# Kernel tuning notes

Measured on AMD Instinct MI355X. Metric: run time of the kernel, lower is better.

## Reference

```python
import jax, jax.numpy as jnp
import numpy as np

MD = 4                  # corr_md
D = 2 * MD + 1          # patch_size = 9


def setup_inputs() -> dict:
    key = jax.random.key(0)
    k1, k2 = jax.random.split(key)
    b, c, h, w = 4, 128, 128, 256
    t1 = jax.random.normal(k1, (b, c, h, w), dtype=jnp.float32)
    t2 = jax.random.normal(k2, (b, c, h, w), dtype=jnp.float32)
    return {"t1": t1, "t2": t2}


def reference(t1, t2):
    # Local cost volume: for each displacement (di, dj) in [-MD, MD]^2,
    # out[b, p, y, x] = sum_c t1[b, c, y, x] * t2[b, c, y+di, x+dj]
    # with zero padding outside t2 (SpatialCorrelationSampler semantics,
    # kernel_size=1, stride=1, dilation_patch=1; no channel normalization).
    b, c, h, w = t1.shape
    t2p = jnp.pad(t2, ((0, 0), (0, 0), (MD, MD), (MD, MD)))
    # Loop over the fixed 9x9 displacement grid (81 small reductions);
    outs = [
        jnp.einsum('bchw,bchw->bhw', t1, t2p[:, :, i:i + h, j:j + w])
        for i in range(D) for j in range(D)
    ]
    return jnp.stack(outs, axis=1)  # [b, 81, h, w]
```

## Files before the change

### kernel.cpp

```cpp
#include <hip/hip_runtime.h>

#define NP 81
#define CC 128
#define HH 128
#define WW 256
#define TX 64

typedef __attribute__((ext_vector_type(8))) short short8;
typedef __attribute__((ext_vector_type(4))) float f32x4;

__device__ __forceinline__ short f2bf(float f) {
    unsigned int u = __builtin_bit_cast(unsigned int, f);
    u += 0x7fffu + ((u >> 16) & 1u);
    return (short)(u >> 16);
}

__global__ __launch_bounds__(256) void corr_mfma_kernel(
        const float* __restrict__ t1, const float* __restrict__ t2,
        float* __restrict__ out) {
    const int id = blockIdx.x;
    const int xt = id & 3;
    const int y  = (id >> 2) & (HH - 1);
    const int b  = id >> 9;
    const int X0 = xt * TX;

    const int tid  = threadIdx.x;
    const int lane = tid & 63;
    const int wv   = tid >> 6;
    const int n    = lane & 15;
    const int q    = lane >> 4;

    __shared__ short smem[2560 + 28800];
    short* sA = smem;
    short* sB = smem + 2560;

    f32x4 acc[9][2];
#pragma unroll
    for (int i = 0; i < 9; i++)
#pragma unroll
        for (int t = 0; t < 2; t++) acc[i][t] = (f32x4){0.f, 0.f, 0.f, 0.f};

    const size_t plane = (size_t)HH * WW;
    const float* t1b = t1 + (size_t)b * CC * plane + (size_t)y * WW;
    const float* t2b = t2 + (size_t)b * CC * plane;

    for (int c0 = 0; c0 < CC; c0 += 32) {
        __syncthreads();
        {
            const int x  = tid & 63;
            const int cg = tid >> 6;
            const float* p = t1b + (size_t)(c0 + cg * 8) * plane + X0 + x;
            short8 pk;
#pragma unroll
            for (int j = 0; j < 8; j++) pk[j] = f2bf(p[(size_t)j * plane]);
            *(short8*)&sA[x * 40 + cg * 8] = pk;
        }
#pragma unroll
        for (int i = 0; i < 12; i++) {
            const int u = tid + i * 256;
            if (u < 2880) {
                const int r   = u / 320;
                const int rem = u - r * 320;
                const int cg  = rem / 80;
                const int ix  = rem - cg * 80;
                const int y2  = y + r - 4;
                const int x2  = X0 - 4 + ix;
                short8 pk;
                if (y2 >= 0 && y2 < HH && x2 >= 0 && x2 < WW) {
                    const float* p = t2b + (size_t)(c0 + cg * 8) * plane
                                   + (size_t)y2 * WW + x2;
#pragma unroll
                    for (int j = 0; j < 8; j++) pk[j] = f2bf(p[(size_t)j * plane]);
                } else {
#pragma unroll
                    for (int j = 0; j < 8; j++) pk[j] = 0;
                }
                *(short8*)&sB[r * 3200 + ix * 40 + cg * 8] = pk;
            }
        }
        __syncthreads();
        const short8 af = *(const short8*)&sA[(16 * wv + n) * 40 + q * 8];
#pragma unroll
        for (int di = 0; di < 9; di++) {
#pragma unroll
            for (int t = 0; t < 2; t++) {
                const short8 bf = *(const short8*)
                    &sB[di * 3200 + (16 * wv + 16 * t + n) * 40 + q * 8];
                acc[di][t] = __builtin_amdgcn_mfma_f32_16x16x32_bf16(
                    af, bf, acc[di][t], 0, 0, 0);
            }
        }
    }

    __syncthreads();
    float* obuf = (float*)smem;
#pragma unroll
    for (int di = 0; di < 9; di++)
#pragma unroll
        for (int t = 0; t < 2; t++)
#pragma unroll
            for (int r = 0; r < 4; r++) {
                const int m  = q * 4 + r;
                const int dj = n - m + 16 * t;
                if (dj >= 0 && dj <= 8)
                    obuf[(di * 9 + dj) * 68 + 16 * wv + m] = acc[di][t][r];
            }
    __syncthreads();
    float* ob = out + (size_t)b * NP * plane + (size_t)y * WW + X0;
#pragma unroll
    for (int i = 0; i < 6; i++) {
        const int u = tid + i * 256;
        if (u < 1296) {
            const int p  = u >> 4;
            const int xu = u & 15;
            f32x4 v = *(const f32x4*)&obuf[p * 68 + xu * 4];
            *(f32x4*)&ob[(size_t)p * plane + xu * 4] = v;
        }
    }
}

extern "C" void kernel_launch(void* const* d_in, const int* in_sizes, int n_in,
                              void* d_out, int out_size, void* d_ws, size_t ws_size,
                              hipStream_t stream) {
    const float* t1 = (const float*)d_in[0];
    const float* t2 = (const float*)d_in[1];
    float* out = (float*)d_out;
    corr_mfma_kernel<<<2048, 256, 0, stream>>>(t1, t2, out);
}
```

Before: 235.2 us.

## Prepack padded bf16 t2 in workspace and use 32x32 MFMA correlation kernel

Adds a prepass that converts t2 to bf16 once into a zero-padded, channel-group-interleaved workspace layout. A new correlation kernel then reads that layout with vector loads, with one row displacement per wave over 9 waves. It uses 32x32x16 bf16 MFMA on 32-pixel tiles and prefetches the next channel chunk into registers before the synchronised LDS store. This removes the repeated fp32-to-bf16 conversion and the halo/boundary logic from the main loop, at the cost of an extra kernel launch and a ~40MB workspace round trip. The old kernel remains as a fallback when the workspace is too small.

```diff
diff --git a/kernel.cpp b/kernel.cpp
--- a/kernel.cpp
+++ b/kernel.cpp
@@ -4,15 +4,122 @@
 #define CC 128
 #define HH 128
 #define WW 256
-#define TX 64
+#define YP 136
+#define XP 288
+#define WS_NEED 40108032ull
 
 typedef __attribute__((ext_vector_type(8))) short short8;
 typedef __attribute__((ext_vector_type(4))) float f32x4;
+typedef __attribute__((ext_vector_type(16))) float f32x16;
 
 __device__ __forceinline__ short f2bf(float f) {
     unsigned int u = __builtin_bit_cast(unsigned int, f);
     u += 0x7fffu + ((u >> 16) & 1u);
     return (short)(u >> 16);
+}
+
+__global__ __launch_bounds__(256) void prepass_t2(const float* __restrict__ t2,
+                                                  short* __restrict__ ws) {
+    const int u = blockIdx.x * 256 + threadIdx.x;
+    const int xp = u % XP;
+    const int v  = u / XP;
+    const int yp = v % YP;
+    const int bc = v / YP;
+    const int y2 = yp - 4, x2 = xp - 4;
+    short8 lo = {0,0,0,0,0,0,0,0}, hi = {0,0,0,0,0,0,0,0};
+    if (y2 >= 0 && y2 < HH && x2 >= 0 && x2 < WW) {
+        const int b = bc >> 3, cg = bc & 7;
+        const size_t pl = (size_t)HH * WW;
+        const float* p = t2 + ((size_t)(b * CC + cg * 16) * HH + y2) * WW + x2;
+#pragma unroll
+        for (int j = 0; j < 8; j++) lo[j] = f2bf(p[(size_t)j * pl]);
+#pragma unroll
+        for (int j = 0; j < 8; j++) hi[j] = f2bf(p[(size_t)(j + 8) * pl]);
+    }
+    short* o = ws + (size_t)u * 16;
+    *(short8*)o = lo;
+    *(short8*)(o + 8) = hi;
+}
+
+__global__ __launch_bounds__(576) void corr32_kernel(const float* __restrict__ t1,
+                                                     const short* __restrict__ ws,
+                                                     float* __restrict__ out) {
+    const int id = blockIdx.x;
+    const int xt = id & 7;
+    const int y  = (id >> 3) & (HH - 1);
+    const int b  = id >> 10;
+    const int X0 = xt * 32;
+
+    const int tid  = threadIdx.x;
+    const int lane = tid & 63;
+    const int w    = tid >> 6;
+    const int n    = lane & 31;
+    const int g    = lane >> 5;
+
+    __shared__ short smem[4608 + 9216];
+    short* sA = smem;
+    short* sB = smem + 4608;
+
+    const size_t plane = (size_t)HH * WW;
+
+    if (tid < 512) {
+        const int x = tid & 31, oct = tid >> 5;
+        const float* p = t1 + (size_t)(b * CC + oct * 8) * plane
+                       + (size_t)y * WW + X0 + x;
+        short8 pk;
+#pragma unroll
+        for (int j = 0; j < 8; j++) pk[j] = f2bf(p[(size_t)j * plane]);
+        *(short8*)&sA[x * 144 + oct * 8] = pk;
+    }
+
+    f32x16 accv[2];
+#pragma unroll
+    for (int t = 0; t < 2; ++t)
+#pragma unroll
+        for (int r = 0; r < 16; ++r) accv[t][r] = 0.f;
+
+    const int u0 = tid, u1 = tid + 576;
+    const int r0 = u0 >> 7, s0 = u0 & 127;
+    const int r1 = u1 >> 7, s1 = u1 & 127;
+    const size_t base0 = ((size_t)b * 8 * YP + (y + r0)) * XP + X0;
+    const size_t base1 = ((size_t)b * 8 * YP + (y + r1)) * XP + X0;
+
+    short8 pf0 = *(const short8*)(ws + base0 * 16 + s0 * 8);
+    short8 pf1 = *(const short8*)(ws + base1 * 16 + s1 * 8);
+
+    for (int kc = 0; kc < 8; ++kc) {
+        __syncthreads();
+        *(short8*)&sB[r0 * 1024 + s0 * 8] = pf0;
+        *(short8*)&sB[r1 * 1024 + s1 * 8] = pf1;
+        if (kc < 7) {
+            const size_t adv = (size_t)(kc + 1) * YP * XP * 16;
+            pf0 = *(const short8*)(ws + base0 * 16 + adv + s0 * 8);
+            pf1 = *(const short8*)(ws + base1 * 16 + adv + s1 * 8);
+        }
+        __syncthreads();
+        const short8 af  = *(const short8*)&sA[n * 144 + kc * 16 + g * 8];
+        const short8 bf0 = *(const short8*)&sB[w * 1024 + n * 16 + g * 8];
+        const short8 bf1 = *(const short8*)&sB[w * 1024 + (32 + n) * 16 + g * 8];
+        accv[0] = __builtin_amdgcn_mfma_f32_32x32x16_bf16(af, bf0, accv[0], 0, 0, 0);
+        accv[1] = __builtin_amdgcn_mfma_f32_32x32x16_bf16(af, bf1, accv[1], 0, 0, 0);
+    }
+
+    __syncthreads();
+    float* obuf = (float*)smem;
+#pragma unroll
+    for (int t = 0; t < 2; ++t)
+#pragma unroll
+        for (int r = 0; r < 16; ++r) {
+            const int m  = (r & 3) + 8 * (r >> 2) + 4 * g;
+            const int dj = n - m + 32 * t;
+            if (dj >= 0 && dj <= 8) obuf[(w * 9 + dj) * 40 + m] = accv[t][r];
+        }
+    __syncthreads();
+    for (int u = tid; u < 648; u += 576) {
+        const int p = u >> 3, xq = u & 7;
+        f32x4 v = *(const f32x4*)&obuf[p * 40 + xq * 4];
+        *(f32x4*)&out[((size_t)(b * NP + p) * HH + y) * WW + X0 + xq * 4] = v;
+    }
 }
 
 __global__ __launch_bounds__(256) void corr_mfma_kernel(
@@ -22,28 +129,23 @@
     const int xt = id & 3;
     const int y  = (id >> 2) & (HH - 1);
     const int b  = id >> 9;
-    const int X0 = xt * TX;
-
+    const int X0 = xt * 64;
     const int tid  = threadIdx.x;
     const int lane = tid & 63;
     const int wv   = tid >> 6;
     const int n    = lane & 15;
     const int q    = lane >> 4;
-
     __shared__ short smem[2560 + 28800];
     short* sA = smem;
     short* sB = smem + 2560;
-
     f32x4 acc[9][2];
 #pragma unroll
     for (int i = 0; i < 9; i++)
 #pragma unroll
         for (int t = 0; t < 2; t++) acc[i][t] = (f32x4){0.f, 0.f, 0.f, 0.f};
-
     const size_t plane = (size_t)HH * WW;
     const float* t1b = t1 + (size_t)b * CC * plane + (size_t)y * WW;
     const float* t2b = t2 + (size_t)b * CC * plane;
-
     for (int c0 = 0; c0 < CC; c0 += 32) {
         __syncthreads();
         {
@@ -91,7 +193,6 @@
             }
         }
     }
-
     __syncthreads();
     float* obuf = (float*)smem;
 #pragma unroll
@@ -125,5 +226,11 @@
     const float* t1 = (const float*)d_in[0];
     const float* t2 = (const float*)d_in[1];
     float* out = (float*)d_out;
-    corr_mfma_kernel<<<2048, 256, 0, stream>>>(t1, t2, out);
-}
+    if (ws_size >= WS_NEED) {
+        short* ws = (short*)d_ws;
+        prepass_t2<<<4896, 256, 0, stream>>>(t2, ws);
+        corr32_kernel<<<4096, 576, 0, stream>>>(t1, ws, out);
+    } else {
+        corr_mfma_kernel<<<2048, 256, 0, stream>>>(t1, t2, out);
+    }
+}
```

Result: faster. 205.8 us (-12.5%).

## Pre-convert t2 to padded bf16 channel-blocked workspace and use small-tile MFMA kernel

Applied to the files above, without the earlier changes.

Adds a prepass that converts t2 to bf16 once into a zero-padded, channel-interleaved workspace layout. The main kernel then loads MFMA B fragments straight from global memory into registers, with no per-block conversion, LDS staging or boundary checks. It uses 16-pixel tiles with 8192 blocks of 512 threads, one wave per vertical displacement row. This removes the repeated fp32 loads and bf16 conversion of overlapping t2 halos, at the cost of an extra kernel launch, a large workspace write and read, and an uneven workload where wave 0 also handles the ninth row. The original kernel is kept as a fallback when the workspace is too small.

```diff
diff --git a/kernel.cpp b/kernel.cpp
--- a/kernel.cpp
+++ b/kernel.cpp
@@ -4,7 +4,9 @@
 #define CC 128
 #define HH 128
 #define WW 256
-#define TX 64
+#define YP 136
+#define XP 288
+#define WS_NEED 40108032ull
 
 typedef __attribute__((ext_vector_type(8))) short short8;
 typedef __attribute__((ext_vector_type(4))) float f32x4;
@@ -13,6 +15,118 @@
     unsigned int u = __builtin_bit_cast(unsigned int, f);
     u += 0x7fffu + ((u >> 16) & 1u);
     return (short)(u >> 16);
+}
+
+__global__ __launch_bounds__(256) void prepass_t2(const float* __restrict__ t2,
+                                                  short* __restrict__ ws) {
+    const int u  = blockIdx.x * 256 + threadIdx.x;
+    const int xh = u % 144;
+    const int v  = u / 144;
+    const int yp = v % YP;
+    const int bc = v / YP;
+    const int y2 = yp - 4;
+    const int x2 = xh * 2 - 4;
+    short8 a0 = {0,0,0,0,0,0,0,0}, a1 = a0, b0 = a0, b1 = a0;
+    if (y2 >= 0 && y2 < HH) {
+        const int b = bc >> 3, cg = bc & 7;
+        const size_t pl = (size_t)HH * WW;
+        const float* p = t2 + ((size_t)(b * CC + cg * 16) * HH + y2) * WW + x2;
+        if (x2 >= 0 && x2 < WW) {
+#pragma unroll
+            for (int j = 0; j < 8; j++) { a0[j] = f2bf(p[(size_t)j * pl]);
+                                          a1[j] = f2bf(p[(size_t)(j + 8) * pl]); }
+        }
+        if (x2 + 1 >= 0 && x2 + 1 < WW) {
+#pragma unroll
+            for (int j = 0; j < 8; j++) { b0[j] = f2bf(p[1 + (size_t)j * pl]);
+                                          b1[j] = f2bf(p[1 + (size_t)(j + 8) * pl]); }
+        }
+    }
+    short* o = ws + (size_t)u * 32;
+    *(short8*)(o)      = a0;  *(short8*)(o + 8)  = a1;
+    *(short8*)(o + 16) = b0;  *(short8*)(o + 24) = b1;
+}
+
+__global__ __launch_bounds__(512, 7) void corr16_v3(const float* __restrict__ t1,
+                                                    const short* __restrict__ ws,
+                                                    float* __restrict__ out) {
+    const int id = blockIdx.x;
+    const int xt = id & 15;
+    const int y  = (id >> 4) & (HH - 1);
+    const int b  = id >> 11;
+    const int X0 = xt * 16;
+
+    const int tid  = threadIdx.x;
+    const int lane = tid & 63;
+    const int w    = tid >> 6;
+    const int nl   = lane & 15;
+    const int q    = lane >> 4;
+
+    __shared__ short sA[16 * 128];
+    __shared__ float obuf[NP * 24];
+
+    const size_t plane = (size_t)HH * WW;
+
+    if (tid < 256) {
+        const int x = tid & 15, oct = tid >> 4;
+        const float* p = t1 + ((size_t)(b * CC + oct * 8) * HH + y) * WW + X0 + x;
+        short8 pk;
+#pragma unroll
+        for (int j = 0; j < 8; j++) pk[j] = f2bf(p[(size_t)j * plane]);
+        *(short8*)&sA[x * 128 + ((oct ^ x) * 8)] = pk;
+    }
+
+    const size_t cs = (size_t)YP * XP * 16;
+    const size_t rb_lane = (size_t)(q >> 1) * cs
+                         + (size_t)(X0 + nl) * 16 + (q & 1) * 8;
+
+    int di = w;
+    size_t rowb = ((size_t)(b * 8) * YP + (y + di)) * XP * 16 + rb_lane;
+
+    short8 B0[4], B1[4];
+#pragma unroll
+    for (int kc = 0; kc < 4; ++kc) {
+        B0[kc] = *(const short8*)(ws + rowb + (size_t)kc * 2 * cs);
+        B1[kc] = *(const short8*)(ws + rowb + (size_t)kc * 2 * cs + 256);
+    }
+
+    __syncthreads();
+
+    const int ntask = (w == 0) ? 2 : 1;
+    for (int pass = 0; pass < ntask; ++pass) {
+        f32x4 a0 = {0.f, 0.f, 0.f, 0.f}, a1 = {0.f, 0.f, 0.f, 0.f};
+#pragma unroll
+        for (int kc = 0; kc < 4; ++kc) {
+            const short8 af = *(const short8*)
+                &sA[nl * 128 + (((kc * 4 + q) ^ nl) * 8)];
+            a0 = __builtin_amdgcn_mfma_f32_16x16x32_bf16(af, B0[kc], a0, 0, 0, 0);
+            a1 = __builtin_amdgcn_mfma_f32_16x16x32_bf16(af, B1[kc], a1, 0, 0, 0);
+        }
+#pragma unroll
+        for (int r = 0; r < 4; ++r) {
+            const int m  = q * 4 + r;
+            const int d0 = nl - m;
+            const int d1 = nl - m + 16;
+            if (d0 >= 0 && d0 <= 8) obuf[(di * 9 + d0) * 24 + m] = a0[r];
+            if (d1 <= 8)            obuf[(di * 9 + d1) * 24 + m] = a1[r];
+        }
+        if (pass + 1 < ntask) {
+            di = 8;
+            rowb = ((size_t)(b * 8) * YP + (y + 8)) * XP * 16 + rb_lane;
+#pragma unroll
+            for (int kc = 0; kc < 4; ++kc) {
+                B0[kc] = *(const short8*)(ws + rowb + (size_t)kc * 2 * cs);
+                B1[kc] = *(const short8*)(ws + rowb + (size_t)kc * 2 * cs + 256);
+            }
+        }
+    }
+
+    __syncthreads();
+    if (tid < 324) {
+        const int p = tid >> 2, xq = tid & 3;
+        const f32x4 vv = *(const f32x4*)&obuf[p * 24 + xq * 4];
+        *(f32x4*)&out[((size_t)(b * NP + p) * HH + y) * WW + X0 + xq * 4] = vv;
+    }
 }
 
 __global__ __launch_bounds__(256) void corr_mfma_kernel(
@@ -22,28 +136,23 @@
     const int xt = id & 3;
     const int y  = (id >> 2) & (HH - 1);
     const int b  = id >> 9;
-    const int X0 = xt * TX;
-
+    const int X0 = xt * 64;
     const int tid  = threadIdx.x;
     const int lane = tid & 63;
     const int wv   = tid >> 6;
     const int n    = lane & 15;
     const int q    = lane >> 4;
-
     __shared__ short smem[2560 + 28800];
     short* sA = smem;
     short* sB = smem + 2560;
-
     f32x4 acc[9][2];
 #pragma unroll
     for (int i = 0; i < 9; i++)
 #pragma unroll
         for (int t = 0; t < 2; t++) acc[i][t] = (f32x4){0.f, 0.f, 0.f, 0.f};
-
     const size_t plane = (size_t)HH * WW;
     const float* t1b = t1 + (size_t)b * CC * plane + (size_t)y * WW;
     const float* t2b = t2 + (size_t)b * CC * plane;
-
     for (int c0 = 0; c0 < CC; c0 += 32) {
         __syncthreads();
         {
@@ -91,7 +200,6 @@
             }
         }
     }
-
     __syncthreads();
     float* obuf = (float*)smem;
 #pragma unroll
@@ -125,5 +233,11 @@
     const float* t1 = (const float*)d_in[0];
     const float* t2 = (const float*)d_in[1];
     float* out = (float*)d_out;
-    corr_mfma_kernel<<<2048, 256, 0, stream>>>(t1, t2, out);
-}
+    if (ws_size >= WS_NEED) {
+        short* ws = (short*)d_ws;
+        prepass_t2<<<2448, 256, 0, stream>>>(t2, ws);
+        corr16_v3<<<8192, 512, 0, stream>>>(t1, ws, out);
+    } else {
+        corr_mfma_kernel<<<2048, 256, 0, stream>>>(t1, t2, out);
+    }
+}
```

Measured after the change: 252.8 us. +7.5%, slower.
